# Optimization experiments

Measured on AMD Instinct MI355X. Metric: run time of the kernel, lower is better.

The kernel has to match this reference:

```python
import jax, jax.numpy as jnp
import numpy as np


def setup_inputs() -> dict:
    key = jax.random.key(0)
    k1, k2 = jax.random.split(key)
    B, N, M, D = 8, 8192, 8192, 3
    input1 = jax.random.normal(k1, (B, N, D), dtype=jnp.float32)
    input2 = jax.random.normal(k2, (B, M, D), dtype=jnp.float32)
    return {"input1": input1, "input2": input2}


def reference(input1, input2):
    # input1: [B, N, 3], input2: [B, M, 3]
    # Squared pairwise distances via ||x||^2 + ||y||^2 - 2<x,y>
    sq1 = jnp.sum(input1 * input1, axis=-1)          # [B, N]
    sq2 = jnp.sum(input2 * input2, axis=-1)          # [B, M]
    inner = jnp.einsum('bnd,bmd->bnm', input1, input2)  # [B, N, M]
    d = sq1[:, :, None] + sq2[:, None, :] - 2.0 * inner  # [B, N, M]
    d = jnp.maximum(d, 0.0)  # numerical guard
    dist1 = jnp.min(d, axis=2)  # [B, N] NN in input2 for each point of input1
    dist2 = jnp.min(d, axis=1)  # [B, M] NN in input1 for each point of input2
    loss = jnp.mean(dist1) + jnp.mean(dist2)
    return loss
```

## Files before the change

kernel.cpp:

```cpp
#include <hip/hip_runtime.h>


typedef _Float16 half8 __attribute__((ext_vector_type(8)));
typedef float    f16x  __attribute__((ext_vector_type(16)));

constexpr int B      = 8;
constexpr int NPTS   = 8192;
constexpr int TOTAL  = B * NPTS;
constexpr int NSTRIP = 256;
constexpr int MHALF  = 4096;
constexpr int CHUNK  = 512;

__device__ __forceinline__ float colmin16(const f16x& a)
{
    float m0 = fminf(fminf(a[0],  a[1]),  a[2]);
    float m1 = fminf(fminf(a[3],  a[4]),  a[5]);
    float m2 = fminf(fminf(a[6],  a[7]),  a[8]);
    float m3 = fminf(fminf(a[9],  a[10]), a[11]);
    float m4 = fminf(fminf(a[12], a[13]), a[14]);
    return fminf(fminf(fminf(m0, m1), m2), fminf(fminf(m3, m4), a[15]));
}

__global__ __launch_bounds__(512, 4) void chamfer_mfma(
    const float* __restrict__ in1, const float* __restrict__ in2,
    float* __restrict__ d1p, float* __restrict__ d2p, float* __restrict__ out)
{
    const int b     = blockIdx.z;
    const int strip = blockIdx.x;
    const int mh    = blockIdx.y;
    const int wave  = threadIdx.x >> 6;
    const int lane  = threadIdx.x & 63;
    const int col   = lane & 31;
    const int half  = lane >> 5;

    if ((blockIdx.x | blockIdx.y | blockIdx.z) == 0 && threadIdx.x == 0)
        *out = 0.0f;

    __shared__ _Float16 ldsB[CHUNK * 16];
    __shared__ unsigned d2lds[MHALF];

    for (int i = threadIdx.x; i < MHALF; i += 512)
        d2lds[i] = 0xFFFFFFFFu;

    const int nbase = strip * NSTRIP + wave * 32;
    half8 afrag;
    {
        const float* a = in1 + ((size_t)b * NPTS + nbase + col) * 3;
        float x = a[0], y = a[1], z = a[2];
        float sq = fmaf(x, x, fmaf(y, y, z * z));
        _Float16 xh = (_Float16)x, yh = (_Float16)y, zh = (_Float16)z;
        _Float16 xl = (_Float16)(x - (float)xh);
        _Float16 yl = (_Float16)(y - (float)yh);
        _Float16 zl = (_Float16)(z - (float)zh);
        _Float16 sh = (_Float16)sq, sl = (_Float16)(sq - (float)sh);
        half8 lo = {xh, yh, zh, xl, yl, zl, xh, yh};
        half8 hi = {zh, sh, sl, (_Float16)1.f, (_Float16)1.f,
                    (_Float16)0.f, (_Float16)0.f, (_Float16)0.f};
        afrag = half ? hi : lo;
    }

    f16x MN1, zero;
#pragma unroll
    for (int r = 0; r < 16; ++r) { MN1[r] = 1e30f; zero[r] = 0.0f; }

    const float* Craw = in2 + ((size_t)b * NPTS + mh * MHALF) * 3;

    for (int c = 0; c < MHALF / CHUNK; ++c) {
        __syncthreads();
        {
            const float* cp = Craw + (size_t)(c * CHUNK + threadIdx.x) * 3;
            float cx = cp[0], cy = cp[1], cz = cp[2];
            float x = -2.f * cx, y = -2.f * cy, z = -2.f * cz;
            float sq = fmaf(cx, cx, fmaf(cy, cy, cz * cz));
            _Float16 xh = (_Float16)x, yh = (_Float16)y, zh = (_Float16)z;
            _Float16 xl = (_Float16)(x - (float)xh);
            _Float16 yl = (_Float16)(y - (float)yh);
            _Float16 zl = (_Float16)(z - (float)zh);
            _Float16 sh = (_Float16)sq, sl = (_Float16)(sq - (float)sh);
            half8 lo = {xh, yh, zh, xh, yh, zh, xl, yl};
            half8 hi = {zl, (_Float16)1.f, (_Float16)1.f, sh, sl,
                        (_Float16)0.f, (_Float16)0.f, (_Float16)0.f};
            *(half8*)&ldsB[threadIdx.x * 16]     = lo;
            *(half8*)&ldsB[threadIdx.x * 16 + 8] = hi;
        }
        __syncthreads();

#pragma unroll 2
        for (int t = 0; t < CHUNK / 32; t += 2) {
            half8 bfA = *(const half8*)&ldsB[((t    ) * 32 + col) * 16 + half * 8];
            half8 bfB = *(const half8*)&ldsB[((t + 1) * 32 + col) * 16 + half * 8];
            f16x accA = __builtin_amdgcn_mfma_f32_32x32x16_f16(afrag, bfA, zero, 0, 0, 0);
            f16x accB = __builtin_amdgcn_mfma_f32_32x32x16_f16(afrag, bfB, zero, 0, 0, 0);

#pragma unroll
            for (int r = 0; r < 16; ++r)
                MN1[r] = fminf(fminf(MN1[r], accA[r]), accB[r]);

            float vA = fmaxf(colmin16(accA), 0.0f);
            atomicMin(&d2lds[c * CHUNK + t * 32 + col], __float_as_uint(vA));
            float vB = fmaxf(colmin16(accB), 0.0f);
            atomicMin(&d2lds[c * CHUNK + (t + 1) * 32 + col], __float_as_uint(vB));
        }
    }
    __syncthreads();

    float* d2 = d2p + ((size_t)b * 32 + strip) * NPTS + mh * MHALF;
    for (int i = threadIdx.x; i < MHALF; i += 512)
        d2[i] = __uint_as_float(d2lds[i]);

#pragma unroll
    for (int m = 1; m <= 16; m <<= 1)
#pragma unroll
        for (int r = 0; r < 16; ++r)
            MN1[r] = fminf(MN1[r], __shfl_xor(MN1[r], m, 64));
    if (col == 0) {
        float* d1 = d1p + ((size_t)b * 2 + mh) * NPTS + nbase;
#pragma unroll
        for (int r = 0; r < 16; ++r)
            d1[(r & 3) + 8 * (r >> 2) + 4 * half] = MN1[r];
    }
}

__global__ __launch_bounds__(256) void reduce_kernel(
    const float* __restrict__ d1p, const float* __restrict__ d2p,
    float* __restrict__ out)
{
    int g  = blockIdx.x * 256 + threadIdx.x;
    int b  = g >> 11;
    int mq = g & 2047;

    const float4* p2 = (const float4*)(d2p + (size_t)b * 32 * NPTS) + mq;
    float4 v2 = p2[0];
#pragma unroll
    for (int s = 1; s < 32; ++s) {
        float4 t = p2[(size_t)s * (NPTS / 4)];
        v2.x = fminf(v2.x, t.x); v2.y = fminf(v2.y, t.y);
        v2.z = fminf(v2.z, t.z); v2.w = fminf(v2.w, t.w);
    }
    float4 a0 = ((const float4*)(d1p + ((size_t)b * 2 + 0) * NPTS))[mq];
    float4 a1 = ((const float4*)(d1p + ((size_t)b * 2 + 1) * NPTS))[mq];
    float v = fmaxf(fminf(a0.x, a1.x), 0.0f) + fmaxf(fminf(a0.y, a1.y), 0.0f)
            + fmaxf(fminf(a0.z, a1.z), 0.0f) + fmaxf(fminf(a0.w, a1.w), 0.0f)
            + v2.x + v2.y + v2.z + v2.w;

#pragma unroll
    for (int off = 32; off; off >>= 1)
        v += __shfl_down(v, off, 64);
    __shared__ float wsum[4];
    int lane = threadIdx.x & 63, w = threadIdx.x >> 6;
    if (lane == 0) wsum[w] = v;
    __syncthreads();
    if (threadIdx.x == 0)
        atomicAdd(out, (wsum[0] + wsum[1] + wsum[2] + wsum[3]) *
                           (1.0f / (float)TOTAL));
}

extern "C" void kernel_launch(void* const* d_in, const int* in_sizes, int n_in,
                              void* d_out, int out_size, void* d_ws, size_t ws_size,
                              hipStream_t stream)
{
    const float* in1 = (const float*)d_in[0];
    const float* in2 = (const float*)d_in[1];
    float* out = (float*)d_out;

    char* ws = (char*)d_ws;
    float* d1p = (float*)ws;
    float* d2p = (float*)(ws + (size_t)2 * TOTAL * 4);

    chamfer_mfma<<<dim3(NPTS / NSTRIP, 2, B), 512, 0, stream>>>(
        in1, in2, d1p, d2p, out);
    reduce_kernel<<<TOTAL / 1024, 256, 0, stream>>>(d1p, d2p, out);
}
```

Before: 93.34 us.

## Replace LDS atomicMin column reduction with per-wave buffers and reshape grid

Measured after the change: 105.9 us. 1.13x slower.

```diff
diff --git a/kernel.cpp b/kernel.cpp
--- a/kernel.cpp
+++ b/kernel.cpp
@@ -4,12 +4,15 @@
 typedef _Float16 half8 __attribute__((ext_vector_type(8)));
 typedef float    f16x  __attribute__((ext_vector_type(16)));
 
-constexpr int B      = 8;
-constexpr int NPTS   = 8192;
-constexpr int TOTAL  = B * NPTS;
-constexpr int NSTRIP = 256;
-constexpr int MHALF  = 4096;
-constexpr int CHUNK  = 512;
+constexpr int B       = 8;
+constexpr int NPTS    = 8192;
+constexpr int TOTAL   = B * NPTS;
+constexpr int NSTRIP  = 128;
+constexpr int NSTRIPS = NPTS / NSTRIP;
+constexpr int MH      = 4;
+constexpr int MHALF   = NPTS / MH;
+constexpr int CHUNK   = 512;
+constexpr int NWAVE   = 4;
 
 __device__ __forceinline__ float colmin16(const f16x& a)
 {
@@ -21,7 +24,7 @@
     return fminf(fminf(fminf(m0, m1), m2), fminf(fminf(m3, m4), a[15]));
 }
 
-__global__ __launch_bounds__(512, 4) void chamfer_mfma(
+__global__ __launch_bounds__(256, 5) void chamfer_mfma(
     const float* __restrict__ in1, const float* __restrict__ in2,
     float* __restrict__ d1p, float* __restrict__ d2p, float* __restrict__ out)
 {
@@ -37,10 +40,7 @@
         *out = 0.0f;
 
     __shared__ _Float16 ldsB[CHUNK * 16];
-    __shared__ unsigned d2lds[MHALF];
-
-    for (int i = threadIdx.x; i < MHALF; i += 512)
-        d2lds[i] = 0xFFFFFFFFu;
+    __shared__ float    d2w[NWAVE][CHUNK];
 
     const int nbase = strip * NSTRIP + wave * 32;
     half8 afrag;
@@ -64,11 +64,14 @@
     for (int r = 0; r < 16; ++r) { MN1[r] = 1e30f; zero[r] = 0.0f; }
 
     const float* Craw = in2 + ((size_t)b * NPTS + mh * MHALF) * 3;
+    float* d2 = d2p + ((size_t)b * NSTRIPS + strip) * NPTS + mh * MHALF;
 
     for (int c = 0; c < MHALF / CHUNK; ++c) {
         __syncthreads();
-        {
-            const float* cp = Craw + (size_t)(c * CHUNK + threadIdx.x) * 3;
+#pragma unroll
+        for (int s = 0; s < 2; ++s) {
+            const int i = threadIdx.x + s * 256;
+            const float* cp = Craw + (size_t)(c * CHUNK + i) * 3;
             float cx = cp[0], cy = cp[1], cz = cp[2];
             float x = -2.f * cx, y = -2.f * cy, z = -2.f * cz;
             float sq = fmaf(cx, cx, fmaf(cy, cy, cz * cz));
@@ -80,8 +83,17 @@
             half8 lo = {xh, yh, zh, xh, yh, zh, xl, yl};
             half8 hi = {zl, (_Float16)1.f, (_Float16)1.f, sh, sl,
                         (_Float16)0.f, (_Float16)0.f, (_Float16)0.f};
-            *(half8*)&ldsB[threadIdx.x * 16]     = lo;
-            *(half8*)&ldsB[threadIdx.x * 16 + 8] = hi;
+            *(half8*)&ldsB[i * 16]     = lo;
+            *(half8*)&ldsB[i * 16 + 8] = hi;
+        }
+        if (c > 0) {
+#pragma unroll
+            for (int s = 0; s < 2; ++s) {
+                const int i = threadIdx.x + s * 256;
+                float v = fminf(fminf(d2w[0][i], d2w[1][i]),
+                                fminf(d2w[2][i], d2w[3][i]));
+                d2[(c - 1) * CHUNK + i] = fmaxf(v, 0.0f);
+            }
         }
         __syncthreads();
 
@@ -94,19 +106,23 @@
 
 #pragma unroll
             for (int r = 0; r < 16; ++r)
-                MN1[r] = fminf(fminf(MN1[r], accA[r]), accB[r]);
+                MN1[r] = fminf(fminf(accA[r], accB[r]), MN1[r]);
 
-            float vA = fmaxf(colmin16(accA), 0.0f);
-            atomicMin(&d2lds[c * CHUNK + t * 32 + col], __float_as_uint(vA));
-            float vB = fmaxf(colmin16(accB), 0.0f);
-            atomicMin(&d2lds[c * CHUNK + (t + 1) * 32 + col], __float_as_uint(vB));
+            float vA = colmin16(accA);
+            float vB = colmin16(accB);
+            vA = fminf(vA, __shfl_xor(vA, 32, 64));
+            vB = fminf(vB, __shfl_xor(vB, 32, 64));
+            d2w[wave][t * 32 + lane] = half ? vB : vA;
         }
     }
     __syncthreads();
-
-    float* d2 = d2p + ((size_t)b * 32 + strip) * NPTS + mh * MHALF;
-    for (int i = threadIdx.x; i < MHALF; i += 512)
-        d2[i] = __uint_as_float(d2lds[i]);
+#pragma unroll
+    for (int s = 0; s < 2; ++s) {
+        const int i = threadIdx.x + s * 256;
+        float v = fminf(fminf(d2w[0][i], d2w[1][i]),
+                        fminf(d2w[2][i], d2w[3][i]));
+        d2[(MHALF / CHUNK - 1) * CHUNK + i] = fmaxf(v, 0.0f);
+    }
 
 #pragma unroll
     for (int m = 1; m <= 16; m <<= 1)
@@ -114,45 +130,46 @@
         for (int r = 0; r < 16; ++r)
             MN1[r] = fminf(MN1[r], __shfl_xor(MN1[r], m, 64));
     if (col == 0) {
-        float* d1 = d1p + ((size_t)b * 2 + mh) * NPTS + nbase;
+        float* d1 = d1p + ((size_t)b * MH + mh) * NPTS + nbase;
 #pragma unroll
         for (int r = 0; r < 16; ++r)
             d1[(r & 3) + 8 * (r >> 2) + 4 * half] = MN1[r];
     }
 }
 
-__global__ __launch_bounds__(256) void reduce_kernel(
+__global__ __launch_bounds__(64) void reduce_kernel(
     const float* __restrict__ d1p, const float* __restrict__ d2p,
     float* __restrict__ out)
 {
-    int g  = blockIdx.x * 256 + threadIdx.x;
+    int g  = blockIdx.x * 64 + threadIdx.x;
     int b  = g >> 11;
     int mq = g & 2047;
 
-    const float4* p2 = (const float4*)(d2p + (size_t)b * 32 * NPTS) + mq;
+    const float4* p2 = (const float4*)(d2p + (size_t)b * NSTRIPS * NPTS) + mq;
     float4 v2 = p2[0];
-#pragma unroll
-    for (int s = 1; s < 32; ++s) {
+#pragma unroll 8
+    for (int s = 1; s < NSTRIPS; ++s) {
         float4 t = p2[(size_t)s * (NPTS / 4)];
         v2.x = fminf(v2.x, t.x); v2.y = fminf(v2.y, t.y);
         v2.z = fminf(v2.z, t.z); v2.w = fminf(v2.w, t.w);
     }
-    float4 a0 = ((const float4*)(d1p + ((size_t)b * 2 + 0) * NPTS))[mq];
-    float4 a1 = ((const float4*)(d1p + ((size_t)b * 2 + 1) * NPTS))[mq];
-    float v = fmaxf(fminf(a0.x, a1.x), 0.0f) + fmaxf(fminf(a0.y, a1.y), 0.0f)
-            + fmaxf(fminf(a0.z, a1.z), 0.0f) + fmaxf(fminf(a0.w, a1.w), 0.0f)
+    const float4* p1 = (const float4*)(d1p + (size_t)b * MH * NPTS) + mq;
+    float4 a = p1[0];
+#pragma unroll
+    for (int s = 1; s < MH; ++s) {
+        float4 t = p1[(size_t)s * (NPTS / 4)];
+        a.x = fminf(a.x, t.x); a.y = fminf(a.y, t.y);
+        a.z = fminf(a.z, t.z); a.w = fminf(a.w, t.w);
+    }
+    float v = fmaxf(a.x, 0.0f) + fmaxf(a.y, 0.0f)
+            + fmaxf(a.z, 0.0f) + fmaxf(a.w, 0.0f)
             + v2.x + v2.y + v2.z + v2.w;
 
 #pragma unroll
     for (int off = 32; off; off >>= 1)
         v += __shfl_down(v, off, 64);
-    __shared__ float wsum[4];
-    int lane = threadIdx.x & 63, w = threadIdx.x >> 6;
-    if (lane == 0) wsum[w] = v;
-    __syncthreads();
     if (threadIdx.x == 0)
-        atomicAdd(out, (wsum[0] + wsum[1] + wsum[2] + wsum[3]) *
-                           (1.0f / (float)TOTAL));
+        atomicAdd(out, v * (1.0f / (float)TOTAL));
 }
 
 extern "C" void kernel_launch(void* const* d_in, const int* in_sizes, int n_in,
@@ -165,9 +182,9 @@
 
     char* ws = (char*)d_ws;
     float* d1p = (float*)ws;
-    float* d2p = (float*)(ws + (size_t)2 * TOTAL * 4);
+    float* d2p = (float*)(ws + (size_t)MH * TOTAL * 4);
 
-    chamfer_mfma<<<dim3(NPTS / NSTRIP, 2, B), 512, 0, stream>>>(
+    chamfer_mfma<<<dim3(NSTRIPS, MH, B), 256, 0, stream>>>(
         in1, in2, d1p, d2p, out);
-    reduce_kernel<<<TOTAL / 1024, 256, 0, stream>>>(d1p, d2p, out);
+    reduce_kernel<<<TOTAL / 4 / 64, 64, 0, stream>>>(d1p, d2p, out);
 }
```
